# Optimization experiments

Measured on AMD Instinct MI355X. Metric: run time of the kernel, lower is better.

Reference implementation:

```python
import jax, jax.numpy as jnp
import numpy as np

N = 8192
D_IN = 256
D_OUT = 256
DROP_P = 0.5


def setup_inputs() -> dict:
    key = jax.random.key(0)
    k1, k2, k3, k4, k5 = jax.random.split(key, 5)
    inputs = jax.random.normal(k1, (N, D_IN), dtype=jnp.float32)
    # torch nn.Linear weights are [d_out, d_in], applied as x @ W.T
    Wq = jax.random.normal(k2, (D_OUT, D_IN), dtype=jnp.float32) * (1.0 / np.sqrt(D_IN))
    Wk = jax.random.normal(k3, (D_OUT, D_IN), dtype=jnp.float32) * (1.0 / np.sqrt(D_IN))
    Wv = jax.random.normal(k4, (D_OUT, D_IN), dtype=jnp.float32) * (1.0 / np.sqrt(D_IN))
    # deterministic dropout keep-mask (True = keep), p=0.5
    drop_mask = jax.random.bernoulli(k5, 1.0 - DROP_P, (N, N))
    return {"inputs": inputs, "Wq": Wq, "Wk": Wk, "Wv": Wv, "drop_mask": drop_mask}


def reference(inputs, Wq, Wk, Wv, drop_mask):
    # QKV projections (no bias)
    q = inputs @ Wq.T  # [N, d_out]
    k = inputs @ Wk.T  # [N, d_out]
    v = inputs @ Wv.T  # [N, d_out]

    d_k = k.shape[1]
    scores = q @ k.T  # [N, N]

    # causal mask: strictly-upper-triangular entries -> -inf
    n = scores.shape[0]
    causal = jnp.triu(jnp.ones((n, n), dtype=bool), k=1)
    masked = jnp.where(causal, -jnp.inf, scores)

    attn_weights = jax.nn.softmax(masked / jnp.sqrt(jnp.float32(d_k)), axis=-1)

    # dropout p=0.5 in train mode: zero dropped entries, scale kept by 1/(1-p)
    scale = jnp.float32(1.0 / (1.0 - DROP_P))
    attn_weights = jnp.where(drop_mask, attn_weights * scale, 0.0)

    context_vector = attn_weights @ v  # [N, d_out]
    return context_vector
```

## Files before the change

kernel.cpp:

```cpp
#include <hip/hip_runtime.h>

#define NT 8192
#define DM 256

typedef float f32x16 __attribute__((ext_vector_type(16)));
typedef float f32x4 __attribute__((ext_vector_type(4)));
typedef __bf16 bf16x8 __attribute__((ext_vector_type(8)));
typedef unsigned int u32x4 __attribute__((ext_vector_type(4)));

#define MFMA32(a, b, c) __builtin_amdgcn_mfma_f32_32x32x16_bf16((a), (b), (c), 0, 0, 0)
#define MFMA16(a, b, c) __builtin_amdgcn_mfma_f32_16x16x32_bf16((a), (b), (c), 0, 0, 0)
#define NEG_INF (-__builtin_inff())

static __device__ __forceinline__ unsigned short f2bf_bits(float f) {
  return __builtin_bit_cast(unsigned short, (__bf16)f);
}
static __device__ __forceinline__ float exp2_fast(float x) {
  return __builtin_amdgcn_exp2f(x);
}
static __device__ __forceinline__ void gload_lds16(const void* g, void* l) {
  __builtin_amdgcn_global_load_lds(
      (const __attribute__((address_space(1))) unsigned int*)g,
      (__attribute__((address_space(3))) unsigned int*)l, 16, 0, 0);
}

__global__ __launch_bounds__(256) void maskpack_kernel(
    const void* __restrict__ mask, unsigned long long* __restrict__ bm) {
  const int t = threadIdx.x, lane = t & 63, w = t >> 6;
  const int r = blockIdx.x + (w << 11);
  const unsigned int* md = (const unsigned int*)mask;
  bool a01 = true, af = true;
#pragma unroll
  for (int k = 0; k < 4; ++k) {
    unsigned int v = md[lane + 64 * k];
    a01 = a01 && (v <= 1u);
    af = af && (v == 0u || v == 0x3F800000u);
  }
  const bool dword_mode = __all(a01) || __all(af);
  unsigned long long* out = bm + (size_t)r * 128;
  if (dword_mode) {
    const unsigned int* mk = (const unsigned int*)mask + (size_t)r * NT;
    const int iters = (r >> 8) + 1;
    for (int it = 0; it < iters; ++it) {
      const int j0 = it * 256;
      unsigned int v0 = mk[j0 + lane];
      unsigned int v1 = mk[j0 + 64 + lane];
      unsigned int v2 = mk[j0 + 128 + lane];
      unsigned int v3 = mk[j0 + 192 + lane];
      unsigned long long b0 = __ballot(v0 != 0u);
      unsigned long long b1 = __ballot(v1 != 0u);
      unsigned long long b2 = __ballot(v2 != 0u);
      unsigned long long b3 = __ballot(v3 != 0u);
      if (lane == 0) {
        out[(j0 >> 6) + 0] = b0;
        out[(j0 >> 6) + 1] = b1;
        out[(j0 >> 6) + 2] = b2;
        out[(j0 >> 6) + 3] = b3;
      }
    }
  } else {
    const unsigned char* mk = (const unsigned char*)mask + (size_t)r * NT;
    unsigned short* outs = (unsigned short*)out;
    const int iters = (r >> 10) + 1;
    for (int it = 0; it < iters; ++it) {
      const uint4 d = *(const uint4*)(mk + it * 1024 + lane * 16);
      unsigned int dws[4] = {d.x, d.y, d.z, d.w};
      unsigned int m16 = 0;
#pragma unroll
      for (int k = 0; k < 4; ++k) {
        unsigned int x = dws[k];
        x |= x >> 4;
        x |= x >> 2;
        x |= x >> 1;
        x &= 0x01010101u;
        m16 |= ((x * 0x01020408u) >> 24) << (4 * k);
      }
      outs[it * 64 + lane] = (unsigned short)m16;
    }
  }
}

__global__ __launch_bounds__(256) void proj_kernel(
    const float* __restrict__ X, const float* __restrict__ Wq,
    const float* __restrict__ Wk, const float* __restrict__ Wv,
    unsigned short* __restrict__ Qs, unsigned short* __restrict__ Kb,
    unsigned short* __restrict__ Vt) {
  __shared__ __align__(16) unsigned short Xs[64 * 256];
  __shared__ __align__(16) unsigned short Ws[64 * 256];
  __shared__ float Tr[4][32 * 33];
  const int ib = blockIdx.x, mat = blockIdx.y;
  const float* W = (mat == 0) ? Wq : (mat == 1) ? Wk : Wv;
  const float wscale = (mat == 0) ? 0.09016844005556021f : (mat == 2 ? 2.0f : 1.0f);
  const int t = threadIdx.x;
  const int lane = t & 63, w = t >> 6;
  const int m = lane & 31, half = lane >> 5;
  const int i0 = ib * 64;
#pragma unroll
  for (int cc = 0; cc < 8; ++cc) {
    int chunk = t + 256 * cc;
    int rr = chunk >> 5, c = chunk & 31;
    const float4* src = (const float4*)(X + (size_t)(i0 + rr) * 256 + c * 8);
    float4 f0 = src[0], f1 = src[1];
    bf16x8 v;
    v[0] = (__bf16)f0.x; v[1] = (__bf16)f0.y; v[2] = (__bf16)f0.z; v[3] = (__bf16)f0.w;
    v[4] = (__bf16)f1.x; v[5] = (__bf16)f1.y; v[6] = (__bf16)f1.z; v[7] = (__bf16)f1.w;
    *(bf16x8*)&Xs[(rr * 32 + (c ^ (rr & 31))) * 8] = v;
  }
  const int wr = w >> 1, wc = w & 1;
  for (int cb = 0; cb < 4; ++cb) {
    __syncthreads();
#pragma unroll
    for (int cc = 0; cc < 8; ++cc) {
      int chunk = t + 256 * cc;
      int rr = chunk >> 5, c = chunk & 31;
      const float4* src = (const float4*)(W + (size_t)(cb * 64 + rr) * 256 + c * 8);
      float4 f0 = src[0], f1 = src[1];
      bf16x8 v;
      v[0] = (__bf16)(f0.x * wscale); v[1] = (__bf16)(f0.y * wscale);
      v[2] = (__bf16)(f0.z * wscale); v[3] = (__bf16)(f0.w * wscale);
      v[4] = (__bf16)(f1.x * wscale); v[5] = (__bf16)(f1.y * wscale);
      v[6] = (__bf16)(f1.z * wscale); v[7] = (__bf16)(f1.w * wscale);
      *(bf16x8*)&Ws[(rr * 32 + (c ^ (rr & 31))) * 8] = v;
    }
    __syncthreads();
    f32x16 acc = {};
    const int ar = 32 * wr + m;
    const int br = 32 * wc + m;
#pragma unroll
    for (int st = 0; st < 16; ++st) {
      int kc = st * 2 + half;
      bf16x8 a = *(const bf16x8*)&Xs[(ar * 32 + (kc ^ (ar & 31))) * 8];
      bf16x8 b = *(const bf16x8*)&Ws[(br * 32 + (kc ^ (br & 31))) * 8];
      acc = MFMA32(a, b, acc);
    }
    if (mat < 2) {
      unsigned short* O = mat ? Kb : Qs;
#pragma unroll
      for (int r = 0; r < 16; ++r) {
        int row = i0 + 32 * wr + (r & 3) + 8 * (r >> 2) + 4 * half;
        int col = cb * 64 + 32 * wc + m;
        O[(size_t)row * DM + col] = f2bf_bits(acc[r]);
      }
    } else {
      float* T = Tr[w];
#pragma unroll
      for (int r = 0; r < 16; ++r) {
        int rl = (r & 3) + 8 * (r >> 2) + 4 * half;
        T[m * 33 + rl] = acc[r];
      }
      asm volatile("s_waitcnt lgkmcnt(0)" ::: "memory");
#pragma unroll
      for (int q = 0; q < 16; ++q) {
        int dl = 2 * q + half;
        float val = T[dl * 33 + m];
        Vt[(size_t)(cb * 64 + 32 * wc + dl) * NT + i0 + 32 * wr + m] = f2bf_bits(val);
      }
      asm volatile("s_waitcnt lgkmcnt(0)" ::: "memory");
    }
  }
}

static __device__ __forceinline__ bf16x8 pack_butterfly(const f32x4 sA, const f32x4 sB,
                                                        unsigned int bits, int q) {
  unsigned int A0, A1, B0, B1;
  {
    unsigned int bbA = bits >> (q * 4);
    unsigned int bbB = bits >> (16 + q * 4);
    float a0 = (bbA & 1u) ? sA[0] : 0.f, a1 = (bbA & 2u) ? sA[1] : 0.f;
    float a2 = (bbA & 4u) ? sA[2] : 0.f, a3 = (bbA & 8u) ? sA[3] : 0.f;
    float b0 = (bbB & 1u) ? sB[0] : 0.f, b1 = (bbB & 2u) ? sB[1] : 0.f;
    float b2 = (bbB & 4u) ? sB[2] : 0.f, b3 = (bbB & 8u) ? sB[3] : 0.f;
    A0 = (unsigned)f2bf_bits(a0) | ((unsigned)f2bf_bits(a1) << 16);
    A1 = (unsigned)f2bf_bits(a2) | ((unsigned)f2bf_bits(a3) << 16);
    B0 = (unsigned)f2bf_bits(b0) | ((unsigned)f2bf_bits(b1) << 16);
    B1 = (unsigned)f2bf_bits(b2) | ((unsigned)f2bf_bits(b3) << 16);
  }
  unsigned int own0 = (q & 2) ? B0 : A0, own1 = (q & 2) ? B1 : A1;
  unsigned int t0 = (q & 2) ? A0 : B0, t1 = (q & 2) ? A1 : B1;
  unsigned int r10 = __shfl_xor(t0, 32);
  unsigned int r11 = __shfl_xor(t1, 32);
  const bool selOwn = ((q ^ (q >> 1)) & 1) != 0;
  unsigned int s20 = selOwn ? own0 : r10;
  unsigned int s21 = selOwn ? own1 : r11;
  unsigned int r20 = __shfl_xor(s20, 16);
  unsigned int r21 = __shfl_xor(s21, 16);
  unsigned int lo0 = (q == 0) ? A0 : (q == 2) ? r10 : r20;
  unsigned int lo1 = (q == 0) ? A1 : (q == 2) ? r11 : r21;
  unsigned int hi0 = (q == 3) ? B0 : (q == 1) ? r10 : r20;
  unsigned int hi1 = (q == 3) ? B1 : (q == 1) ? r11 : r21;
  return __builtin_bit_cast(bf16x8, (u32x4){lo0, lo1, hi0, hi1});
}

__global__ __launch_bounds__(256, 2) void flash_kernel(
    const unsigned short* __restrict__ Qs, const unsigned short* __restrict__ Kg,
    const unsigned short* __restrict__ Vtg, const unsigned long long* __restrict__ bm,
    float* __restrict__ ml_out, unsigned short* __restrict__ acc_out) {
  __shared__ __align__(16) unsigned short Ksh[64 * 256];
  __shared__ __align__(16) unsigned short Vsh[256 * 64];
  const int ib = blockIdx.x;
  const int seg = blockIdx.y;
  const int jb_end = ib + 1;
  const int jb0 = seg * 8;
  if (jb0 >= jb_end) return;
  const int jb1 = (jb0 + 8 < jb_end) ? jb0 + 8 : jb_end;
  const int t = threadIdx.x, lane = t & 63, w = t >> 6;
  const int m = lane & 15, q = lane >> 4;
  const int i0 = ib * 64, rw0 = i0 + 16 * w;
  const int myrow = rw0 + m;

  bf16x8 qf[8];
  {
    const unsigned short* qp = Qs + (size_t)myrow * DM + q * 8;
#pragma unroll
    for (int st = 0; st < 8; ++st) qf[st] = *(const bf16x8*)(qp + st * 32);
  }
  f32x4 oacc[16] = {};
  float mrun = -1e30f, lrun = 0.f;

#define STAGE(JB)                                                             \
  {                                                                           \
    const int j64_ = (JB) * 64;                                               \
    _Pragma("unroll") for (int i_ = 0; i_ < 8; ++i_) {                        \
      int chunk = t + 256 * i_;                                               \
      int row = chunk >> 5, slot = chunk & 31;                                \
      gload_lds16(Kg + (size_t)(j64_ + row) * DM + (slot ^ (row & 31)) * 8,   \
                  Ksh + (size_t)chunk * 8);                                   \
    }                                                                         \
    _Pragma("unroll") for (int i_ = 0; i_ < 8; ++i_) {                        \
      int chunk = t + 256 * i_;                                               \
      int d_ = chunk >> 3, slot = chunk & 7;                                  \
      gload_lds16(Vtg + (size_t)d_ * NT + j64_ + (slot ^ (d_ & 7)) * 8,       \
                  Vsh + (size_t)chunk * 8);                                   \
    }                                                                         \
  }

  STAGE(jb0)
  unsigned long long bits = bm[(size_t)myrow * 128 + jb0];
  for (int jb = jb0; jb < jb1; ++jb) {
    const int j64 = jb * 64;
    __syncthreads();
    if (j64 <= rw0 + 15) {
      f32x4 s[4] = {};
#pragma unroll
      for (int st = 0; st < 8; ++st) {
        int kc = st * 4 + q;
#pragma unroll
        for (int ct = 0; ct < 4; ++ct) {
          int jr = ct * 16 + m;
          bf16x8 a = *(const bf16x8*)&Ksh[(jr * 32 + (kc ^ (jr & 31))) * 8];
          s[ct] = MFMA16(a, qf[st], s[ct]);
        }
      }
      if (j64 + 63 > rw0) {
#pragma unroll
        for (int ct = 0; ct < 4; ++ct)
#pragma unroll
          for (int r = 0; r < 4; ++r)
            if (j64 + ct * 16 + q * 4 + r > myrow) s[ct][r] = NEG_INF;
      }
      float mx = fmaxf(fmaxf(fmaxf(s[0][0], s[0][1]), fmaxf(s[0][2], s[0][3])),
                       fmaxf(fmaxf(s[1][0], s[1][1]), fmaxf(s[1][2], s[1][3])));
      mx = fmaxf(mx, fmaxf(fmaxf(fmaxf(s[2][0], s[2][1]), fmaxf(s[2][2], s[2][3])),
                           fmaxf(fmaxf(s[3][0], s[3][1]), fmaxf(s[3][2], s[3][3]))));
      mx = fmaxf(mx, __shfl_xor(mx, 16));
      mx = fmaxf(mx, __shfl_xor(mx, 32));
      const float mn = fmaxf(mrun, mx);
#pragma unroll
      for (int ct = 0; ct < 4; ++ct)
#pragma unroll
        for (int r = 0; r < 4; ++r) s[ct][r] = exp2_fast(s[ct][r] - mn);
      float rs = ((s[0][0] + s[0][1]) + (s[0][2] + s[0][3])) +
                 ((s[1][0] + s[1][1]) + (s[1][2] + s[1][3])) +
                 ((s[2][0] + s[2][1]) + (s[2][2] + s[2][3])) +
                 ((s[3][0] + s[3][1]) + (s[3][2] + s[3][3]));
      rs += __shfl_xor(rs, 16);
      rs += __shfl_xor(rs, 32);
      if (__all(mn == mrun)) {
        lrun += rs;
      } else {
        float alpha = exp2_fast(mrun - mn);
        lrun = lrun * alpha + rs;
#pragma unroll
        for (int ct = 0; ct < 16; ++ct)
#pragma unroll
          for (int r = 0; r < 4; ++r) oacc[ct][r] *= alpha;
        mrun = mn;
      }
      bf16x8 pf0 = pack_butterfly(s[0], s[1], (unsigned int)bits, q);
      bf16x8 pf1 = pack_butterfly(s[2], s[3], (unsigned int)(bits >> 32), q);
#pragma unroll
      for (int ct = 0; ct < 16; ++ct) {
        int d = ct * 16 + m;
        bf16x8 a0 = *(const bf16x8*)&Vsh[(d * 8 + (q ^ (d & 7))) * 8];
        bf16x8 a1 = *(const bf16x8*)&Vsh[(d * 8 + ((q + 4) ^ (d & 7))) * 8];
        oacc[ct] = MFMA16(a0, pf0, oacc[ct]);
        oacc[ct] = MFMA16(a1, pf1, oacc[ct]);
      }
    }
    __syncthreads();
    if (jb + 1 < jb1) {
      STAGE(jb + 1)
      bits = bm[(size_t)myrow * 128 + jb + 1];
    }
  }
#undef STAGE
  const int a_ = ib >> 3, r_ = ib & 7;
  const int g = 4 * a_ * (a_ + 1) + r_ * (a_ + 1) + seg;
  if (q == 0) {
    float* mlb = ml_out + ((size_t)g * 64 + 16 * w + m) * 2;
    mlb[0] = mrun;
    mlb[1] = lrun;
  }
  unsigned short* ab = acc_out + ((size_t)g * 64 + 16 * w + m) * DM;
#pragma unroll
  for (int ct = 0; ct < 16; ++ct) {
    unsigned long long pk = 0;
#pragma unroll
    for (int r = 0; r < 4; ++r)
      pk |= (unsigned long long)f2bf_bits(oacc[ct][r]) << (16 * r);
    *(unsigned long long*)&ab[ct * 16 + q * 4] = pk;
  }
}

__global__ __launch_bounds__(256) void combine_kernel(
    const float* __restrict__ ml, const unsigned short* __restrict__ pacc,
    float* __restrict__ out) {
  const int t = threadIdx.x;
  const int row = blockIdx.x * 32 + (t >> 3);
  const int cg = (t & 7) * 32;
  const int ib = row >> 6, rib = row & 63;
  const int a = ib >> 3, r = ib & 7;
  const int g0 = 4 * a * (a + 1) + r * (a + 1);
  const int ns = a + 1;
  float M = -1e30f;
  for (int s = 0; s < ns; ++s) M = fmaxf(M, ml[((size_t)(g0 + s) * 64 + rib) * 2]);
  float Wd = 0.f;
  float acc[32];
#pragma unroll
  for (int j = 0; j < 32; ++j) acc[j] = 0.f;
  for (int s = 0; s < ns; ++s) {
    const float* mls = ml + ((size_t)(g0 + s) * 64 + rib) * 2;
    float wv = exp2_fast(mls[0] - M);
    Wd += wv * mls[1];
    const unsigned short* pa = pacc + ((size_t)(g0 + s) * 64 + rib) * DM + cg;
#pragma unroll
    for (int v4 = 0; v4 < 4; ++v4) {
      bf16x8 b = *(const bf16x8*)(pa + v4 * 8);
#pragma unroll
      for (int j = 0; j < 8; ++j) acc[v4 * 8 + j] += wv * (float)b[j];
    }
  }
  float inv = 1.0f / Wd;
#pragma unroll
  for (int j = 0; j < 32; ++j) out[(size_t)row * DM + cg + j] = acc[j] * inv;
}

extern "C" void kernel_launch(void* const* d_in, const int* in_sizes, int n_in,
                              void* d_out, int out_size, void* d_ws, size_t ws_size,
                              hipStream_t stream) {
  const float* X  = (const float*)d_in[0];
  const float* Wq = (const float*)d_in[1];
  const float* Wk = (const float*)d_in[2];
  const float* Wv = (const float*)d_in[3];
  const void* mask = d_in[4];
  float* out = (float*)d_out;

  char* ws = (char*)d_ws;
  unsigned short* Qs = (unsigned short*)(ws + 4096);
  unsigned short* Kb = Qs + (size_t)NT * DM;
  unsigned short* Vt = Kb + (size_t)NT * DM;
  float* ml = (float*)(Vt + (size_t)NT * DM);
  unsigned short* pacc = (unsigned short*)(ml + (size_t)1088 * 64 * 2);
  unsigned long long* bmw = (unsigned long long*)((char*)pacc + (size_t)1088 * 64 * DM * 2);

  maskpack_kernel<<<2048, 256, 0, stream>>>(mask, bmw);
  proj_kernel<<<dim3(128, 3), 256, 0, stream>>>(X, Wq, Wk, Wv, Qs, Kb, Vt);
  flash_kernel<<<dim3(128, 16), 256, 0, stream>>>(Qs, Kb, Vt, bmw, ml, pacc);
  combine_kernel<<<256, 256, 0, stream>>>(ml, pacc, out);
}
```

Baseline: 458.0 us.

## Switch flash kernel to 32x32 MFMA with 2x2 wave split over rows and key columns

The flash attention kernel now uses 32x32x16 bf16 MFMA instead of 16x16x32. Each wave handles 32 query rows and half of each 64-key block, so waves are arranged 2x2 over rows and key columns rather than four 16-row strips. Each wave keeps its own running max and sum, which doubles the partial outputs written to the workspace and the number of segments the combine kernel has to merge. The aim is fewer MFMA issues and LDS fragment reads per tile and a simpler P repack, at the cost of more partial-output traffic and a more expensive combine step.

Result: slower. 655.6 us (+43.2%).

```diff
diff --git a/kernel.cpp b/kernel.cpp
--- a/kernel.cpp
+++ b/kernel.cpp
@@ -160,40 +160,9 @@
   }
 }
 
-static __device__ __forceinline__ bf16x8 pack_butterfly(const f32x4 sA, const f32x4 sB,
-                                                        unsigned int bits, int q) {
-  unsigned int A0, A1, B0, B1;
-  {
-    unsigned int bbA = bits >> (q * 4);
-    unsigned int bbB = bits >> (16 + q * 4);
-    float a0 = (bbA & 1u) ? sA[0] : 0.f, a1 = (bbA & 2u) ? sA[1] : 0.f;
-    float a2 = (bbA & 4u) ? sA[2] : 0.f, a3 = (bbA & 8u) ? sA[3] : 0.f;
-    float b0 = (bbB & 1u) ? sB[0] : 0.f, b1 = (bbB & 2u) ? sB[1] : 0.f;
-    float b2 = (bbB & 4u) ? sB[2] : 0.f, b3 = (bbB & 8u) ? sB[3] : 0.f;
-    A0 = (unsigned)f2bf_bits(a0) | ((unsigned)f2bf_bits(a1) << 16);
-    A1 = (unsigned)f2bf_bits(a2) | ((unsigned)f2bf_bits(a3) << 16);
-    B0 = (unsigned)f2bf_bits(b0) | ((unsigned)f2bf_bits(b1) << 16);
-    B1 = (unsigned)f2bf_bits(b2) | ((unsigned)f2bf_bits(b3) << 16);
-  }
-  unsigned int own0 = (q & 2) ? B0 : A0, own1 = (q & 2) ? B1 : A1;
-  unsigned int t0 = (q & 2) ? A0 : B0, t1 = (q & 2) ? A1 : B1;
-  unsigned int r10 = __shfl_xor(t0, 32);
-  unsigned int r11 = __shfl_xor(t1, 32);
-  const bool selOwn = ((q ^ (q >> 1)) & 1) != 0;
-  unsigned int s20 = selOwn ? own0 : r10;
-  unsigned int s21 = selOwn ? own1 : r11;
-  unsigned int r20 = __shfl_xor(s20, 16);
-  unsigned int r21 = __shfl_xor(s21, 16);
-  unsigned int lo0 = (q == 0) ? A0 : (q == 2) ? r10 : r20;
-  unsigned int lo1 = (q == 0) ? A1 : (q == 2) ? r11 : r21;
-  unsigned int hi0 = (q == 3) ? B0 : (q == 1) ? r10 : r20;
-  unsigned int hi1 = (q == 3) ? B1 : (q == 1) ? r11 : r21;
-  return __builtin_bit_cast(bf16x8, (u32x4){lo0, lo1, hi0, hi1});
-}
-
 __global__ __launch_bounds__(256, 2) void flash_kernel(
     const unsigned short* __restrict__ Qs, const unsigned short* __restrict__ Kg,
-    const unsigned short* __restrict__ Vtg, const unsigned long long* __restrict__ bm,
+    const unsigned short* __restrict__ Vtg, const unsigned int* __restrict__ bm,
     float* __restrict__ ml_out, unsigned short* __restrict__ acc_out) {
   __shared__ __align__(16) unsigned short Ksh[64 * 256];
   __shared__ __align__(16) unsigned short Vsh[256 * 64];
@@ -204,17 +173,19 @@
   if (jb0 >= jb_end) return;
   const int jb1 = (jb0 + 8 < jb_end) ? jb0 + 8 : jb_end;
   const int t = threadIdx.x, lane = t & 63, w = t >> 6;
-  const int m = lane & 15, q = lane >> 4;
-  const int i0 = ib * 64, rw0 = i0 + 16 * w;
-  const int myrow = rw0 + m;
-
-  bf16x8 qf[8];
+  const int la = lane & 31, h = lane >> 5;
+  const int wr = w >> 1, wc = w & 1;
+  const int i0 = ib * 64, rw0 = i0 + 32 * wr;
+  const int myrow = rw0 + la;
+  const int joff = 32 * wc;
+
+  bf16x8 qf[16];
   {
-    const unsigned short* qp = Qs + (size_t)myrow * DM + q * 8;
-#pragma unroll
-    for (int st = 0; st < 8; ++st) qf[st] = *(const bf16x8*)(qp + st * 32);
-  }
-  f32x4 oacc[16] = {};
+    const unsigned short* qp = Qs + (size_t)myrow * DM + 8 * h;
+#pragma unroll
+    for (int ks = 0; ks < 16; ++ks) qf[ks] = *(const bf16x8*)(qp + ks * 16);
+  }
+  f32x16 oacc[8] = {};
   float mrun = -1e30f, lrun = 0.f;
 
 #define STAGE(JB)                                                             \
@@ -235,45 +206,33 @@
   }
 
   STAGE(jb0)
-  unsigned long long bits = bm[(size_t)myrow * 128 + jb0];
+  unsigned int bits = bm[(size_t)myrow * 256 + jb0 * 2 + wc];
   for (int jb = jb0; jb < jb1; ++jb) {
-    const int j64 = jb * 64;
+    const int j32 = jb * 64 + joff;
     __syncthreads();
-    if (j64 <= rw0 + 15) {
-      f32x4 s[4] = {};
-#pragma unroll
-      for (int st = 0; st < 8; ++st) {
-        int kc = st * 4 + q;
-#pragma unroll
-        for (int ct = 0; ct < 4; ++ct) {
-          int jr = ct * 16 + m;
-          bf16x8 a = *(const bf16x8*)&Ksh[(jr * 32 + (kc ^ (jr & 31))) * 8];
-          s[ct] = MFMA16(a, qf[st], s[ct]);
-        }
-      }
-      if (j64 + 63 > rw0) {
-#pragma unroll
-        for (int ct = 0; ct < 4; ++ct)
-#pragma unroll
-          for (int r = 0; r < 4; ++r)
-            if (j64 + ct * 16 + q * 4 + r > myrow) s[ct][r] = NEG_INF;
-      }
-      float mx = fmaxf(fmaxf(fmaxf(s[0][0], s[0][1]), fmaxf(s[0][2], s[0][3])),
-                       fmaxf(fmaxf(s[1][0], s[1][1]), fmaxf(s[1][2], s[1][3])));
-      mx = fmaxf(mx, fmaxf(fmaxf(fmaxf(s[2][0], s[2][1]), fmaxf(s[2][2], s[2][3])),
-                           fmaxf(fmaxf(s[3][0], s[3][1]), fmaxf(s[3][2], s[3][3]))));
-      mx = fmaxf(mx, __shfl_xor(mx, 16));
+    if (j32 <= rw0 + 31) {
+      f32x16 s = {};
+      const int krow = joff + la;
+#pragma unroll
+      for (int ks = 0; ks < 16; ++ks) {
+        bf16x8 a = *(const bf16x8*)&Ksh[(krow * 32 + ((2 * ks + h) ^ (krow & 31))) * 8];
+        s = MFMA32(a, qf[ks], s);
+      }
+      if (j32 + 31 > rw0) {
+#pragma unroll
+        for (int reg = 0; reg < 16; ++reg)
+          if (j32 + (reg & 3) + 8 * (reg >> 2) + 4 * h > myrow) s[reg] = NEG_INF;
+      }
+      float mx = fmaxf(fmaxf(fmaxf(fmaxf(s[0], s[1]), fmaxf(s[2], s[3])),
+                             fmaxf(fmaxf(s[4], s[5]), fmaxf(s[6], s[7]))),
+                       fmaxf(fmaxf(fmaxf(s[8], s[9]), fmaxf(s[10], s[11])),
+                             fmaxf(fmaxf(s[12], s[13]), fmaxf(s[14], s[15]))));
       mx = fmaxf(mx, __shfl_xor(mx, 32));
       const float mn = fmaxf(mrun, mx);
 #pragma unroll
-      for (int ct = 0; ct < 4; ++ct)
-#pragma unroll
-        for (int r = 0; r < 4; ++r) s[ct][r] = exp2_fast(s[ct][r] - mn);
-      float rs = ((s[0][0] + s[0][1]) + (s[0][2] + s[0][3])) +
-                 ((s[1][0] + s[1][1]) + (s[1][2] + s[1][3])) +
-                 ((s[2][0] + s[2][1]) + (s[2][2] + s[2][3])) +
-                 ((s[3][0] + s[3][1]) + (s[3][2] + s[3][3]));
-      rs += __shfl_xor(rs, 16);
+      for (int reg = 0; reg < 16; ++reg) s[reg] = exp2_fast(s[reg] - mn);
+      float rs = (((s[0] + s[1]) + (s[2] + s[3])) + ((s[4] + s[5]) + (s[6] + s[7]))) +
+                 (((s[8] + s[9]) + (s[10] + s[11])) + ((s[12] + s[13]) + (s[14] + s[15])));
       rs += __shfl_xor(rs, 32);
       if (__all(mn == mrun)) {
         lrun += rs;
@@ -281,45 +240,70 @@
         float alpha = exp2_fast(mrun - mn);
         lrun = lrun * alpha + rs;
 #pragma unroll
-        for (int ct = 0; ct < 16; ++ct)
-#pragma unroll
-          for (int r = 0; r < 4; ++r) oacc[ct][r] *= alpha;
+        for (int dt = 0; dt < 8; ++dt)
+#pragma unroll
+          for (int reg = 0; reg < 16; ++reg) oacc[dt][reg] *= alpha;
         mrun = mn;
       }
-      bf16x8 pf0 = pack_butterfly(s[0], s[1], (unsigned int)bits, q);
-      bf16x8 pf1 = pack_butterfly(s[2], s[3], (unsigned int)(bits >> 32), q);
-#pragma unroll
-      for (int ct = 0; ct < 16; ++ct) {
-        int d = ct * 16 + m;
-        bf16x8 a0 = *(const bf16x8*)&Vsh[(d * 8 + (q ^ (d & 7))) * 8];
-        bf16x8 a1 = *(const bf16x8*)&Vsh[(d * 8 + ((q + 4) ^ (d & 7))) * 8];
-        oacc[ct] = MFMA16(a0, pf0, oacc[ct]);
-        oacc[ct] = MFMA16(a1, pf1, oacc[ct]);
+      unsigned int pd[8];
+#pragma unroll
+      for (int e = 0; e < 8; ++e) {
+        int jb_local = (2 * e & 3) + 8 * (2 * e >> 2) + 4 * h;
+        float v0 = ((bits >> jb_local) & 1u) ? s[2 * e] : 0.f;
+        float v1 = ((bits >> (jb_local + 1)) & 1u) ? s[2 * e + 1] : 0.f;
+        pd[e] = (unsigned)f2bf_bits(v0) | ((unsigned)f2bf_bits(v1) << 16);
+      }
+      bf16x8 pfrag[2];
+#pragma unroll
+      for (int v = 0; v < 2; ++v) {
+        const int eA = 4 * v;
+        unsigned int s0 = h ? pd[eA + 0] : pd[eA + 2];
+        unsigned int s1 = h ? pd[eA + 1] : pd[eA + 3];
+        unsigned int t0 = __shfl_xor(s0, 32);
+        unsigned int t1 = __shfl_xor(s1, 32);
+        unsigned int d0 = h ? t0 : pd[eA + 0];
+        unsigned int d1 = h ? t1 : pd[eA + 1];
+        unsigned int d2 = h ? pd[eA + 2] : t0;
+        unsigned int d3 = h ? pd[eA + 3] : t1;
+        pfrag[v] = __builtin_bit_cast(bf16x8, (u32x4){d0, d1, d2, d3});
+      }
+#pragma unroll
+      for (int dt = 0; dt < 8; ++dt) {
+        const int d = dt * 32 + la;
+#pragma unroll
+        for (int v = 0; v < 2; ++v) {
+          const int o = 4 * wc + 2 * v + h;
+          bf16x8 a = *(const bf16x8*)&Vsh[(d * 8 + (o ^ (d & 7))) * 8];
+          oacc[dt] = MFMA32(a, pfrag[v], oacc[dt]);
+        }
       }
     }
     __syncthreads();
     if (jb + 1 < jb1) {
       STAGE(jb + 1)
-      bits = bm[(size_t)myrow * 128 + jb + 1];
+      bits = bm[(size_t)myrow * 256 + (jb + 1) * 2 + wc];
     }
   }
 #undef STAGE
   const int a_ = ib >> 3, r_ = ib & 7;
-  const int g = 4 * a_ * (a_ + 1) + r_ * (a_ + 1) + seg;
-  if (q == 0) {
-    float* mlb = ml_out + ((size_t)g * 64 + 16 * w + m) * 2;
+  const int g = (4 * a_ * (a_ + 1) + r_ * (a_ + 1) + seg) * 2 + wc;
+  const int rowl = 32 * wr + la;
+  if (h == 0) {
+    float* mlb = ml_out + ((size_t)g * 64 + rowl) * 2;
     mlb[0] = mrun;
     mlb[1] = lrun;
   }
-  unsigned short* ab = acc_out + ((size_t)g * 64 + 16 * w + m) * DM;
-#pragma unroll
-  for (int ct = 0; ct < 16; ++ct) {
-    unsigned long long pk = 0;
-#pragma unroll
-    for (int r = 0; r < 4; ++r)
-      pk |= (unsigned long long)f2bf_bits(oacc[ct][r]) << (16 * r);
-    *(unsigned long long*)&ab[ct * 16 + q * 4] = pk;
-  }
+  unsigned short* ab = acc_out + ((size_t)g * 64 + rowl) * DM;
+#pragma unroll
+  for (int dt = 0; dt < 8; ++dt)
+#pragma unroll
+    for (int rr = 0; rr < 4; ++rr) {
+      unsigned long long pk = 0;
+#pragma unroll
+      for (int r = 0; r < 4; ++r)
+        pk |= (unsigned long long)f2bf_bits(oacc[dt][4 * rr + r]) << (16 * r);
+      *(unsigned long long*)&ab[dt * 32 + 8 * rr + 4 * h] = pk;
+    }
 }
 
 __global__ __launch_bounds__(256) void combine_kernel(
@@ -330,8 +314,8 @@
   const int cg = (t & 7) * 32;
   const int ib = row >> 6, rib = row & 63;
   const int a = ib >> 3, r = ib & 7;
-  const int g0 = 4 * a * (a + 1) + r * (a + 1);
-  const int ns = a + 1;
+  const int g0 = (4 * a * (a + 1) + r * (a + 1)) * 2;
+  const int ns = (a + 1) * 2;
   float M = -1e30f;
   for (int s = 0; s < ns; ++s) M = fmaxf(M, ml[((size_t)(g0 + s) * 64 + rib) * 2]);
   float Wd = 0.f;
@@ -370,11 +354,12 @@
   unsigned short* Kb = Qs + (size_t)NT * DM;
   unsigned short* Vt = Kb + (size_t)NT * DM;
   float* ml = (float*)(Vt + (size_t)NT * DM);
-  unsigned short* pacc = (unsigned short*)(ml + (size_t)1088 * 64 * 2);
-  unsigned long long* bmw = (unsigned long long*)((char*)pacc + (size_t)1088 * 64 * DM * 2);
+  unsigned short* pacc = (unsigned short*)(ml + (size_t)2176 * 64 * 2);
+  unsigned long long* bmw = (unsigned long long*)((char*)pacc + (size_t)2176 * 64 * DM * 2);
 
   maskpack_kernel<<<2048, 256, 0, stream>>>(mask, bmw);
   proj_kernel<<<dim3(128, 3), 256, 0, stream>>>(X, Wq, Wk, Wv, Qs, Kb, Vt);
-  flash_kernel<<<dim3(128, 16), 256, 0, stream>>>(Qs, Kb, Vt, bmw, ml, pacc);
+  flash_kernel<<<dim3(128, 16), 256, 0, stream>>>(Qs, Kb, Vt, (const unsigned int*)bmw,
+                                                  ml, pacc);
   combine_kernel<<<256, 256, 0, stream>>>(ml, pacc, out);
 }
```
